# Kernel optimization log

Hardware: AMD Instinct MI355X
Metric: run time of the kernel (lower is better)

The kernel has to match this reference:

```python
import jax, jax.numpy as jnp
import numpy as np

B, L, H, NH = 2, 1024, 768, 12
NE, M, NC, CW = 24, 3, 2, 8
BLOCK, NCLS = 64, 97
OFFSET = 1  # bert cls offset


def setup_inputs() -> dict:
    key = jax.random.key(0)
    ks = jax.random.split(key, 10)
    s = 0.02
    return {
        "sequence_output": jax.random.normal(ks[0], (B, L, H), jnp.float32),
        "attention": jax.random.uniform(ks[1], (B, NH, L, L), jnp.float32),
        "mention_starts": jax.random.randint(ks[2], (B, NE, M), 0, L - 2),
        "coref_starts": jax.random.randint(ks[3], (B, NE, NC), 0, L - CW),
        "W_head": jax.random.normal(ks[4], (H, 2 * H), jnp.float32) * s,
        "b_head": jnp.zeros((H,), jnp.float32),
        "W_tail": jax.random.normal(ks[5], (H, 2 * H), jnp.float32) * s,
        "b_tail": jnp.zeros((H,), jnp.float32),
        "W_proj": jax.random.normal(ks[6], (H, H * BLOCK), jnp.float32) * s,
        "W_cls": jax.random.normal(ks[7], (NCLS, H), jnp.float32) * s,
        "b_cls": jnp.zeros((NCLS,), jnp.float32),
    }


def reference(sequence_output, attention, mention_starts, coref_starts,
              W_head, b_head, W_tail, b_tail, W_proj, W_cls, b_cls):
    # ---- get_hrt (NoGraphConv/NoKGEmbedding => graph feats are zeros; residual=True) ----
    p = mention_starts + OFFSET                              # [B,NE,M]
    bidx = jnp.arange(B)[:, None, None]
    m_emb = sequence_output[bidx, p]                         # [B,NE,M,H]
    # attention[i,:,pos] gathered for every mention -> [B,NE,M,NH,L]
    m_att = attention[bidx, :, p]

    # gated coref: gate_score = mean-over-mentions, sum-over-heads, normalized
    att = m_att.mean(2).sum(2)                               # [B,NE,L]
    gate = att / att.sum(-1, keepdims=True)                  # [B,NE,L]

    widx = coref_starts[..., None] + jnp.arange(CW)          # [B,NE,NC,CW]
    gate_g = jnp.take_along_axis(gate[:, :, None, :], widx, axis=-1)   # [B,NE,NC,CW]
    seq_g = sequence_output[jnp.arange(B)[:, None, None, None], widx]  # [B,NE,NC,CW,H]
    coref_emb = (gate_g[..., None] * seq_g).sum(3)           # [B,NE,NC,H]

    # entity embedding: logsumexp over mentions + gated coref vectors
    e_emb = jax.nn.logsumexp(jnp.concatenate([m_emb, coref_emb], axis=2), axis=2)  # [B,NE,H]
    e_att = m_att.mean(2)                                    # [B,NE,NH,L]

    # head-tail localized context: relu((h_att*t_att).sum(heads)), normalize, mix tokens
    ht = jax.nn.relu(jnp.einsum('behl,bfhl->befl', e_att, e_att))      # [B,NE,NE,L]
    ht = ht / (ht.sum(-1, keepdims=True) + 1e-10)
    rs = jnp.einsum('befl,bld->befd', ht, sequence_output)   # [B,NE,NE,H]

    hs = jnp.broadcast_to(e_emb[:, :, None, :], (B, NE, NE, H))
    ts = jnp.broadcast_to(e_emb[:, None, :, :], (B, NE, NE, H))

    # ---- extractors + grouped bilinear + projection + classifier ----
    zh = jnp.tanh(jnp.concatenate([hs, rs], -1) @ W_head.T + b_head)   # [B,NE,NE,H]
    zt = jnp.tanh(jnp.concatenate([ts, rs], -1) @ W_tail.T + b_tail)
    K = H // BLOCK
    b1 = zh.reshape(B, NE, NE, K, BLOCK)
    b2 = zt.reshape(B, NE, NE, K, BLOCK)
    bl = (b1[..., :, None] * b2[..., None, :]).reshape(B, NE, NE, H * BLOCK)
    feature = bl @ W_proj.T                                  # [B,NE,NE,H] (NoAxialTransformer adds zeros)
    logits = feature @ W_cls.T + b_cls                       # [B,NE,NE,NCLS]
    return logits
```

## Files before the change

### kernel.cpp

```cpp
#include <hip/hip_runtime.h>
#include <math.h>

#define BB   2
#define LL   1024
#define HH   768
#define NHH  12
#define NEE  24
#define MMM  3
#define NCC  2
#define CWW  8
#define BLK  64
#define NCLS 97
#define KB   12
#define HB   49152
#define NCP  128
#define NCT  7
#define NEF  1152

typedef unsigned int uint;
typedef unsigned short ushort;
typedef __attribute__((ext_vector_type(8))) short bf16x8;
typedef __attribute__((ext_vector_type(4))) float f32x4;

__device__ __forceinline__ ushort f2bf(float f) {
    uint u = __float_as_uint(f);
    u += 0x7fffu + ((u >> 16) & 1u);
    return (ushort)(u >> 16);
}

__global__ void k_eatt(const float* __restrict__ att_in, const int* __restrict__ ms,
                       float* __restrict__ e_att) {
    int blk = blockIdx.x;
    int h = blk % NHH;
    int e = (blk / NHH) % NEE;
    int b = blk / (NHH * NEE);
    int base = (b * NEE + e) * MMM;
    int p0 = ms[base + 0] + 1;
    int p1 = ms[base + 1] + 1;
    int p2 = ms[base + 2] + 1;
    const float* r0 = att_in + ((size_t)(b * NHH + h) * LL + p0) * LL;
    const float* r1 = att_in + ((size_t)(b * NHH + h) * LL + p1) * LL;
    const float* r2 = att_in + ((size_t)(b * NHH + h) * LL + p2) * LL;
    float* o = e_att + ((size_t)(b * NEE + e) * NHH + h) * LL;
    for (int l = threadIdx.x; l < LL; l += blockDim.x)
        o[l] = (r0[l] + r1[l] + r2[l]) * (1.f / 3.f);
}

__global__ void k_gate(const float* __restrict__ e_att, float* __restrict__ gate) {
    int be = blockIdx.x;
    __shared__ float att_s[LL];
    __shared__ float red[4];
    const float* ea = e_att + (size_t)be * NHH * LL;
    float lsum = 0.f;
    for (int l = threadIdx.x; l < LL; l += blockDim.x) {
        float a = 0.f;
        for (int h = 0; h < NHH; h++) a += ea[h * LL + l];
        att_s[l] = a;
        lsum += a;
    }
    for (int off = 32; off; off >>= 1) lsum += __shfl_down(lsum, off, 64);
    if ((threadIdx.x & 63) == 0) red[threadIdx.x >> 6] = lsum;
    __syncthreads();
    float inv = 1.f / (red[0] + red[1] + red[2] + red[3]);
    for (int l = threadIdx.x; l < LL; l += blockDim.x)
        gate[(size_t)be * LL + l] = att_s[l] * inv;
}

__global__ void k_eemb(const float* __restrict__ seq, const float* __restrict__ gate,
                       const int* __restrict__ ms, const int* __restrict__ cs,
                       float* __restrict__ e_emb) {
    int be = blockIdx.x;
    int b = be / NEE;
    int p0 = ms[be * MMM + 0] + 1, p1 = ms[be * MMM + 1] + 1, p2 = ms[be * MMM + 2] + 1;
    int c0 = cs[be * NCC + 0], c1 = cs[be * NCC + 1];
    for (int d = threadIdx.x; d < HH; d += blockDim.x) {
        float v0 = seq[((size_t)b * LL + p0) * HH + d];
        float v1 = seq[((size_t)b * LL + p1) * HH + d];
        float v2 = seq[((size_t)b * LL + p2) * HH + d];
        float s0 = 0.f, s1 = 0.f;
        for (int w = 0; w < CWW; w++) {
            s0 += gate[(size_t)be * LL + c0 + w] * seq[((size_t)b * LL + c0 + w) * HH + d];
            s1 += gate[(size_t)be * LL + c1 + w] * seq[((size_t)b * LL + c1 + w) * HH + d];
        }
        float mx = fmaxf(fmaxf(fmaxf(v0, v1), fmaxf(v2, s0)), s1);
        float s = expf(v0 - mx) + expf(v1 - mx) + expf(v2 - mx) + expf(s0 - mx) + expf(s1 - mx);
        e_emb[(size_t)be * HH + d] = logf(s) + mx;
    }
}

__global__ void k_ht(const float* __restrict__ e_att, float* __restrict__ ht) {
    int blk = blockIdx.x;
    int f = blk % NEE;
    int e = (blk / NEE) % NEE;
    int b = blk / (NEE * NEE);
    const float* ea = e_att + (size_t)(b * NEE + e) * NHH * LL;
    const float* fa = e_att + (size_t)(b * NEE + f) * NHH * LL;
    __shared__ float hts[LL];
    __shared__ float red[4];
    float lsum = 0.f;
    for (int l = threadIdx.x; l < LL; l += blockDim.x) {
        float s = 0.f;
        for (int h = 0; h < NHH; h++) s += ea[h * LL + l] * fa[h * LL + l];
        s = fmaxf(s, 0.f);
        hts[l] = s;
        lsum += s;
    }
    for (int off = 32; off; off >>= 1) lsum += __shfl_down(lsum, off, 64);
    if ((threadIdx.x & 63) == 0) red[threadIdx.x >> 6] = lsum;
    __syncthreads();
    float inv = 1.f / (red[0] + red[1] + red[2] + red[3] + 1e-10f);
    for (int l = threadIdx.x; l < LL; l += blockDim.x)
        ht[(size_t)blk * LL + l] = hts[l] * inv;
}

__global__ void k_zrs(float* __restrict__ rs) {
    int i = blockIdx.x * 256 + threadIdx.x;
    rs[i] = 0.f;
}

__global__ void k_rs(const float* __restrict__ seq, const float* __restrict__ ht,
                     float* __restrict__ rs) {
    int m0 = blockIdx.x * 64;
    int n0 = blockIdx.y * 64;
    int b  = blockIdx.z >> 1;
    int k0base = (blockIdx.z & 1) * 512;
    const float* A  = ht  + (size_t)b * 576 * 1024;
    const float* Bm = seq + (size_t)b * 1024 * 768;
    float* C = rs + (size_t)b * 576 * 768;
    __shared__ float As[16][68], Bs[16][68];
    int tx = threadIdx.x & 15, ty = threadIdx.x >> 4;
    int lr = threadIdx.x >> 2;
    int lk = (threadIdx.x & 3) * 4;
    int kr = threadIdx.x >> 4;
    int c4 = (threadIdx.x & 15) * 4;
    float acc[4][4] = {};
    const float* arow = A + (size_t)(m0 + lr) * 1024 + k0base;
    const float* brow = Bm + (size_t)(k0base + kr) * 768 + n0 + c4;
    for (int k0 = 0; k0 < 512; k0 += 16) {
        float4 av = *(const float4*)(arow + k0 + lk);
        float4 bv = *(const float4*)(brow + (size_t)k0 * 768);
        __syncthreads();
        As[lk + 0][lr] = av.x; As[lk + 1][lr] = av.y; As[lk + 2][lr] = av.z; As[lk + 3][lr] = av.w;
        *(float4*)&Bs[kr][c4] = bv;
        __syncthreads();
#pragma unroll
        for (int kk = 0; kk < 16; kk++) {
            float a0 = As[kk][ty * 4 + 0], a1 = As[kk][ty * 4 + 1];
            float a2 = As[kk][ty * 4 + 2], a3 = As[kk][ty * 4 + 3];
            float b0 = Bs[kk][tx * 4 + 0], b1 = Bs[kk][tx * 4 + 1];
            float b2 = Bs[kk][tx * 4 + 2], b3 = Bs[kk][tx * 4 + 3];
            acc[0][0] += a0 * b0; acc[0][1] += a0 * b1; acc[0][2] += a0 * b2; acc[0][3] += a0 * b3;
            acc[1][0] += a1 * b0; acc[1][1] += a1 * b1; acc[1][2] += a1 * b2; acc[1][3] += a1 * b3;
            acc[2][0] += a2 * b0; acc[2][1] += a2 * b1; acc[2][2] += a2 * b2; acc[2][3] += a2 * b3;
            acc[3][0] += a3 * b0; acc[3][1] += a3 * b1; acc[3][2] += a3 * b2; acc[3][3] += a3 * b3;
        }
    }
#pragma unroll
    for (int i = 0; i < 4; i++)
#pragma unroll
        for (int j = 0; j < 4; j++)
            atomicAdd(&C[(size_t)(m0 + ty * 4 + i) * 768 + n0 + tx * 4 + j], acc[i][j]);
}

__global__ void k_hw(const float* __restrict__ e_emb, const float* __restrict__ Wh,
                     const float* __restrict__ Wt, float* __restrict__ hsW,
                     float* __restrict__ tsW) {
    int m2 = blockIdx.x;
    int which = blockIdx.y;
    int chunk = blockIdx.z;
    const float* Wm = which ? Wt : Wh;
    float* outp = which ? tsW : hsW;
    __shared__ float xs[HH];
    const float* x = e_emb + (size_t)m2 * HH;
    for (int j = threadIdx.x; j < HH; j += 256) xs[j] = x[j];
    __syncthreads();
    int lane = threadIdx.x & 63, w = threadIdx.x >> 6;
    int d0 = chunk * 64 + w * 16;
#pragma unroll 4
    for (int i = 0; i < 16; i++) {
        int d = d0 + i;
        const float* wr = Wm + (size_t)d * (2 * HH);
        float s = 0.f;
#pragma unroll
        for (int jj = 0; jj < 12; jj++) s += xs[lane + jj * 64] * wr[lane + jj * 64];
        for (int off = 32; off; off >>= 1) s += __shfl_down(s, off, 64);
        if (lane == 0) outp[(size_t)m2 * HH + d] = s;
    }
}

__global__ void k_rsw(const float* __restrict__ rs, const float* __restrict__ Wh,
                      const float* __restrict__ Wt, float* __restrict__ rsW) {
    int m0 = blockIdx.x * 64, n0 = blockIdx.y * 64;
    __shared__ float As[16][68], Bs[16][68];
    int tx = threadIdx.x & 15, ty = threadIdx.x >> 4;
    int lr = threadIdx.x >> 2;
    int lk = (threadIdx.x & 3) * 4;
    float acc[4][4] = {};
    int n = n0 + lr;
    const float* brow = (n < HH) ? (Wh + (size_t)n * (2 * HH) + HH)
                                 : (Wt + (size_t)(n - HH) * (2 * HH) + HH);
    const float* arow = rs + (size_t)(m0 + lr) * HH;
    for (int k0 = 0; k0 < HH; k0 += 16) {
        float4 av = *(const float4*)(arow + k0 + lk);
        float4 bv = *(const float4*)(brow + k0 + lk);
        __syncthreads();
        As[lk + 0][lr] = av.x; As[lk + 1][lr] = av.y; As[lk + 2][lr] = av.z; As[lk + 3][lr] = av.w;
        Bs[lk + 0][lr] = bv.x; Bs[lk + 1][lr] = bv.y; Bs[lk + 2][lr] = bv.z; Bs[lk + 3][lr] = bv.w;
        __syncthreads();
#pragma unroll
        for (int kk = 0; kk < 16; kk++) {
            float a0 = As[kk][ty * 4 + 0], a1 = As[kk][ty * 4 + 1];
            float a2 = As[kk][ty * 4 + 2], a3 = As[kk][ty * 4 + 3];
            float b0 = Bs[kk][tx * 4 + 0], b1 = Bs[kk][tx * 4 + 1];
            float b2 = Bs[kk][tx * 4 + 2], b3 = Bs[kk][tx * 4 + 3];
            acc[0][0] += a0 * b0; acc[0][1] += a0 * b1; acc[0][2] += a0 * b2; acc[0][3] += a0 * b3;
            acc[1][0] += a1 * b0; acc[1][1] += a1 * b1; acc[1][2] += a1 * b2; acc[1][3] += a1 * b3;
            acc[2][0] += a2 * b0; acc[2][1] += a2 * b1; acc[2][2] += a2 * b2; acc[2][3] += a2 * b3;
            acc[3][0] += a3 * b0; acc[3][1] += a3 * b1; acc[3][2] += a3 * b2; acc[3][3] += a3 * b3;
        }
    }
#pragma unroll
    for (int i = 0; i < 4; i++)
#pragma unroll
        for (int j = 0; j < 4; j++)
            rsW[(size_t)(m0 + ty * 4 + i) * (2 * HH) + n0 + tx * 4 + j] = acc[i][j];
}

__global__ void k_tanh(const float* __restrict__ rsW, const float* __restrict__ hsW,
                       const float* __restrict__ tsW, const float* __restrict__ bh,
                       const float* __restrict__ bt, ushort* __restrict__ zb) {
    size_t i = (size_t)blockIdx.x * 256 + threadIdx.x;
    if (i >= (size_t)NEF * 2 * HH) return;
    int nn = (int)(i % (2 * HH));
    int m = (int)(i / (2 * HH));
    int f = m % NEE;
    int e = (m / NEE) % NEE;
    int b = m / (NEE * NEE);
    float v = rsW[i];
    if (nn < HH) v = tanhf(v + hsW[(size_t)(b * NEE + e) * HH + nn] + bh[nn]);
    else {
        int d = nn - HH;
        v = tanhf(v + tsW[(size_t)(b * NEE + f) * HH + d] + bt[d]);
    }
    zb[i] = f2bf(v);
}

__global__ void k_wcp(const float* __restrict__ Wc, ushort* __restrict__ wcpack) {
    int t = blockIdx.x * 256 + threadIdx.x;
    if (t >= 24 * NCT * 64) return;
    int kc = t / (NCT * 64);
    int r = t % (NCT * 64);
    int ct = r >> 6;
    int lane = r & 63;
    int c = ct * 16 + (lane & 15);
    int k0 = kc * 32 + (lane >> 4) * 8;
    uint u[4] = {0u, 0u, 0u, 0u};
    if (c < NCLS) {
        const float* src = Wc + (size_t)c * HH + k0;
        float4 f0 = *(const float4*)src;
        float4 f1 = *(const float4*)(src + 4);
        u[0] = (uint)f2bf(f0.x) | ((uint)f2bf(f0.y) << 16);
        u[1] = (uint)f2bf(f0.z) | ((uint)f2bf(f0.w) << 16);
        u[2] = (uint)f2bf(f1.x) | ((uint)f2bf(f1.y) << 16);
        u[3] = (uint)f2bf(f1.z) | ((uint)f2bf(f1.w) << 16);
    }
    *(uint4*)(wcpack + (size_t)t * 8) = make_uint4(u[0], u[1], u[2], u[3]);
}

__global__ void k_wf(const float* __restrict__ Wp, const ushort* __restrict__ wcpack,
                     ushort* __restrict__ bpack) {
    int tid = threadIdx.x;
    int lane = tid & 63, w = tid >> 6;
    int r16 = lane & 15, tt = lane >> 4;
    int n0 = blockIdx.x * 64 + w * 16;
    const float* ap = Wp + (size_t)(tt * 8) * HB + n0 + r16;
    const uint4* wb = (const uint4*)wcpack;

    f32x4 acc[NCT];
    f32x4 zero = {0.f, 0.f, 0.f, 0.f};
#pragma unroll
    for (int ct = 0; ct < NCT; ct++) acc[ct] = zero;

    for (int kc = 0; kc < 24; kc++) {
        const float* a0 = ap + (size_t)(kc * 32) * HB;
        float f[8];
#pragma unroll
        for (int j = 0; j < 8; j++) f[j] = a0[(size_t)j * HB];
        union { bf16x8 v; uint u[4]; } a;
#pragma unroll
        for (int q = 0; q < 4; q++)
            a.u[q] = (__float_as_uint(f[2 * q]) >> 16) |
                     (__float_as_uint(f[2 * q + 1]) & 0xFFFF0000u);
#pragma unroll
        for (int ct = 0; ct < NCT; ct++) {
            union { uint4 q; bf16x8 v; } b;
            b.q = wb[(size_t)(kc * NCT + ct) * 64 + lane];
            acc[ct] = __builtin_amdgcn_mfma_f32_16x16x32_bf16(a.v, b.v, acc[ct], 0, 0, 0);
        }
    }
#pragma unroll
    for (int ct = 0; ct < NCT; ct++) {
        int c = ct * 16 + r16;
#pragma unroll
        for (int r = 0; r < 4; r++) {
            int n = n0 + tt * 4 + r;
            bpack[((size_t)(n >> 3) * NCP + c) * 8 + (n & 7)] = f2bf(acc[ct][r]);
        }
    }
}

__global__ void k_init(float* __restrict__ out, const float* __restrict__ bc) {
    int i = blockIdx.x * 256 + threadIdx.x;
    if (i < NEF * NCLS) out[i] = bc[i % NCLS];
}

#define ZTP 88
#define ZHP 48
__global__ __launch_bounds__(256, 2) void k_logits(const ushort* __restrict__ zb,
                                                   const ushort* __restrict__ bpack,
                                                   float* __restrict__ out) {
    __shared__ ushort zhs[64 * ZHP];
    __shared__ ushort zts[64 * ZTP];
    __shared__ ushort Bls[16384];
    int m0 = blockIdx.x * 64;
    int kb = blockIdx.y;
    int kg = kb >> 1;
    int ihalf = (kb & 1) * 32;
    int tid = threadIdx.x;
    int lane = tid & 63, w = tid >> 6;
    int tt = lane >> 4, r16 = lane & 15;
    int wm = (w & 1) * 32, wn = (w >> 1) * 64;

    {
        int row = tid >> 2, c8 = (tid & 3) * 16;
        const ushort* src = zb + (size_t)(m0 + row) * 1536 + 768 + kg * 64 + c8;
        uint4 v0 = *(const uint4*)src;
        uint4 v1 = *(const uint4*)(src + 8);
        *(uint4*)&zts[row * ZTP + c8] = v0;
        *(uint4*)&zts[row * ZTP + c8 + 8] = v1;
    }
    {
        int row = tid >> 2, c8 = (tid & 3) * 8;
        const ushort* src = zb + (size_t)(m0 + row) * 1536 + kg * 64 + ihalf + c8;
        *(uint4*)&zhs[row * ZHP + c8] = *(const uint4*)src;
    }

    f32x4 acc[2][4];
    f32x4 zero = {0.f, 0.f, 0.f, 0.f};
#pragma unroll
    for (int t = 0; t < 2; t++)
#pragma unroll
        for (int n = 0; n < 4; n++) acc[t][n] = zero;

    const char* bbase = (const char*)bpack + (size_t)kb * 2048 * 256;
    for (int g = 0; g < 16; g++) {
        __syncthreads();
        const char* sb = bbase + (size_t)g * 32768;
#pragma unroll
        for (int q = 0; q < 8; q++) {
            int off = (q * 4 + w) * 1024;
            __builtin_amdgcn_global_load_lds(
                (const __attribute__((address_space(1))) void*)(sb + off + lane * 16),
                (__attribute__((address_space(3))) void*)((char*)Bls + off),
                16, 0, 0);
        }
        __syncthreads();
#pragma unroll
        for (int ks = 0; ks < 4; ks++) {
            int s = g * 4 + ks;
            int il = s >> 1;
            int j0 = (s & 1) * 32;
            bf16x8 af[2];
#pragma unroll
            for (int t = 0; t < 2; t++) {
                int row = wm + t * 16 + r16;
                float zhf = __uint_as_float((uint)zhs[row * ZHP + il] << 16);
                union { bf16x8 v; uint u[4]; } zt8, a;
                zt8.v = *(const bf16x8*)&zts[row * ZTP + j0 + tt * 8];
#pragma unroll
                for (int q = 0; q < 4; q++) {
                    uint p = zt8.u[q];
                    uint lo = __float_as_uint(__uint_as_float(p << 16) * zhf);
                    uint hi = __float_as_uint(__uint_as_float(p & 0xFFFF0000u) * zhf);
                    a.u[q] = (lo >> 16) | (hi & 0xFFFF0000u);
                }
                af[t] = a.v;
            }
#pragma unroll
            for (int n = 0; n < 4; n++) {
                bf16x8 bf = *(const bf16x8*)&Bls[(size_t)((ks * 4 + tt) * NCP + wn + n * 16 + r16) * 8];
                acc[0][n] = __builtin_amdgcn_mfma_f32_16x16x32_bf16(af[0], bf, acc[0][n], 0, 0, 0);
                acc[1][n] = __builtin_amdgcn_mfma_f32_16x16x32_bf16(af[1], bf, acc[1][n], 0, 0, 0);
            }
        }
    }
    int rbase = (lane >> 4) * 4;
#pragma unroll
    for (int t = 0; t < 2; t++)
#pragma unroll
        for (int n = 0; n < 4; n++) {
            int c = wn + n * 16 + r16;
            if (c < NCLS) {
                int row = m0 + wm + t * 16 + rbase;
#pragma unroll
                for (int r = 0; r < 4; r++)
                    atomicAdd(&out[(size_t)(row + r) * NCLS + c], acc[t][n][r]);
            }
        }
}

extern "C" void kernel_launch(void* const* d_in, const int* in_sizes, int n_in,
                              void* d_out, int out_size, void* d_ws, size_t ws_size,
                              hipStream_t stream) {
    const float* seq  = (const float*)d_in[0];
    const float* attn = (const float*)d_in[1];
    const int*   ms   = (const int*)d_in[2];
    const int*   cs   = (const int*)d_in[3];
    const float* Wh   = (const float*)d_in[4];
    const float* bh   = (const float*)d_in[5];
    const float* Wt   = (const float*)d_in[6];
    const float* bt   = (const float*)d_in[7];
    const float* Wp   = (const float*)d_in[8];
    const float* Wc   = (const float*)d_in[9];
    const float* bc   = (const float*)d_in[10];
    float* out = (float*)d_out;

    float* w     = (float*)d_ws;
    float* rsW   = w;
    float* regB  = w + 1769472;
    float* e_att = regB;
    float* gate  = e_att + 589824;
    float* ht    = gate + 49152;
    float* rs    = ht + 1179648;
    float* eemb  = rs + 884736;
    float* hsW   = eemb + 36864;
    float* tsW   = hsW + 36864;
    ushort* bpack  = (ushort*)regB;
    ushort* zb     = (ushort*)(regB + 3145728);
    ushort* wcpack = (ushort*)(regB + 4030464);

    k_wcp<<<(24 * NCT * 64 + 255) / 256, 256, 0, stream>>>(Wc, wcpack);
    k_eatt<<<BB * NEE * NHH, 256, 0, stream>>>(attn, ms, e_att);
    k_gate<<<BB * NEE, 256, 0, stream>>>(e_att, gate);
    k_eemb<<<BB * NEE, 256, 0, stream>>>(seq, gate, ms, cs, eemb);
    k_ht<<<NEF, 256, 0, stream>>>(e_att, ht);
    k_zrs<<<(NEF * HH) / 256, 256, 0, stream>>>(rs);
    k_rs<<<dim3(576 / 64, HH / 64, BB * 2), 256, 0, stream>>>(seq, ht, rs);
    k_hw<<<dim3(48, 2, 12), 256, 0, stream>>>(eemb, Wh, Wt, hsW, tsW);
    k_rsw<<<dim3(NEF / 64, 2 * HH / 64), 256, 0, stream>>>(rs, Wh, Wt, rsW);
    k_tanh<<<(NEF * 2 * HH + 255) / 256, 256, 0, stream>>>(rsW, hsW, tsW, bh, bt, zb);
    k_wf<<<HB / 64, 256, 0, stream>>>(Wp, wcpack, bpack);
    k_init<<<(NEF * NCLS + 255) / 256, 256, 0, stream>>>(out, bc);
    k_logits<<<dim3(NEF / 64, 24), 256, 0, stream>>>(zb, bpack, out);
}
```

Before: 490.4 us.

## Fuse small kernels: prep, head attention/gate/emb, mid GEMMs, tanh epilogue

Merges the weight packing, rs zeroing and output bias init into one launch, and combines mention attention averaging, gate normalisation and entity embedding into a single 1024-thread block per entity. The rs GEMM and the hs/ts projections now share one launch, and the tanh/bias/bf16 conversion moves into the epilogue of the rs-weight GEMM, so the rsW intermediate is never written to memory. This removes launch overhead and the gate and rsW round trips through global memory. In exchange it has fewer launches with mixed block roles, and the head kernel runs only 48 large blocks.

```diff
diff --git a/kernel.cpp b/kernel.cpp
--- a/kernel.cpp
+++ b/kernel.cpp
@@ -28,63 +28,89 @@
     return (ushort)(u >> 16);
 }
 
-__global__ void k_eatt(const float* __restrict__ att_in, const int* __restrict__ ms,
-                       float* __restrict__ e_att) {
-    int blk = blockIdx.x;
-    int h = blk % NHH;
-    int e = (blk / NHH) % NEE;
-    int b = blk / (NHH * NEE);
-    int base = (b * NEE + e) * MMM;
+__global__ void k_prep(const float* __restrict__ Wc, ushort* __restrict__ wcpack,
+                       float* __restrict__ rs, float* __restrict__ out,
+                       const float* __restrict__ bc) {
+    int bid = blockIdx.x;
+    if (bid < 42) {
+        int t = bid * 256 + threadIdx.x;
+        if (t >= 24 * NCT * 64) return;
+        int kc = t / (NCT * 64);
+        int r = t % (NCT * 64);
+        int ct = r >> 6;
+        int lane = r & 63;
+        int c = ct * 16 + (lane & 15);
+        int k0 = kc * 32 + (lane >> 4) * 8;
+        uint u[4] = {0u, 0u, 0u, 0u};
+        if (c < NCLS) {
+            const float* src = Wc + (size_t)c * HH + k0;
+            float4 f0 = *(const float4*)src;
+            float4 f1 = *(const float4*)(src + 4);
+            u[0] = (uint)f2bf(f0.x) | ((uint)f2bf(f0.y) << 16);
+            u[1] = (uint)f2bf(f0.z) | ((uint)f2bf(f0.w) << 16);
+            u[2] = (uint)f2bf(f1.x) | ((uint)f2bf(f1.y) << 16);
+            u[3] = (uint)f2bf(f1.z) | ((uint)f2bf(f1.w) << 16);
+        }
+        *(uint4*)(wcpack + (size_t)t * 8) = make_uint4(u[0], u[1], u[2], u[3]);
+    } else if (bid < 42 + 3456) {
+        int i = (bid - 42) * 256 + threadIdx.x;
+        rs[i] = 0.f;
+    } else {
+        int i = (bid - 3498) * 256 + threadIdx.x;
+        if (i < NEF * NCLS) out[i] = bc[i % NCLS];
+    }
+}
+
+__global__ void k_head(const float* __restrict__ att_in, const float* __restrict__ seq,
+                       const int* __restrict__ ms, const int* __restrict__ cs,
+                       float* __restrict__ e_att, float* __restrict__ e_emb) {
+    __shared__ float es[NHH][LL];
+    __shared__ float gs[LL];
+    __shared__ float red[16];
+    int be = blockIdx.x;
+    int b = be / NEE;
+    int base = be * MMM;
     int p0 = ms[base + 0] + 1;
     int p1 = ms[base + 1] + 1;
     int p2 = ms[base + 2] + 1;
-    const float* r0 = att_in + ((size_t)(b * NHH + h) * LL + p0) * LL;
-    const float* r1 = att_in + ((size_t)(b * NHH + h) * LL + p1) * LL;
-    const float* r2 = att_in + ((size_t)(b * NHH + h) * LL + p2) * LL;
-    float* o = e_att + ((size_t)(b * NEE + e) * NHH + h) * LL;
-    for (int l = threadIdx.x; l < LL; l += blockDim.x)
-        o[l] = (r0[l] + r1[l] + r2[l]) * (1.f / 3.f);
-}
-
-__global__ void k_gate(const float* __restrict__ e_att, float* __restrict__ gate) {
-    int be = blockIdx.x;
-    __shared__ float att_s[LL];
-    __shared__ float red[4];
-    const float* ea = e_att + (size_t)be * NHH * LL;
-    float lsum = 0.f;
-    for (int l = threadIdx.x; l < LL; l += blockDim.x) {
-        float a = 0.f;
-        for (int h = 0; h < NHH; h++) a += ea[h * LL + l];
-        att_s[l] = a;
-        lsum += a;
-    }
-    for (int off = 32; off; off >>= 1) lsum += __shfl_down(lsum, off, 64);
-    if ((threadIdx.x & 63) == 0) red[threadIdx.x >> 6] = lsum;
+    int l = threadIdx.x;
+    float* eo = e_att + (size_t)be * NHH * LL;
+#pragma unroll
+    for (int h = 0; h < NHH; h++) {
+        const float* basep = att_in + (size_t)(b * NHH + h) * LL * LL;
+        float v = (basep[(size_t)p0 * LL + l] + basep[(size_t)p1 * LL + l] +
+                   basep[(size_t)p2 * LL + l]) * (1.f / 3.f);
+        es[h][l] = v;
+        eo[h * LL + l] = v;
+    }
     __syncthreads();
-    float inv = 1.f / (red[0] + red[1] + red[2] + red[3]);
-    for (int l = threadIdx.x; l < LL; l += blockDim.x)
-        gate[(size_t)be * LL + l] = att_s[l] * inv;
-}
-
-__global__ void k_eemb(const float* __restrict__ seq, const float* __restrict__ gate,
-                       const int* __restrict__ ms, const int* __restrict__ cs,
-                       float* __restrict__ e_emb) {
-    int be = blockIdx.x;
-    int b = be / NEE;
-    int p0 = ms[be * MMM + 0] + 1, p1 = ms[be * MMM + 1] + 1, p2 = ms[be * MMM + 2] + 1;
-    int c0 = cs[be * NCC + 0], c1 = cs[be * NCC + 1];
-    for (int d = threadIdx.x; d < HH; d += blockDim.x) {
+    float a = 0.f;
+#pragma unroll
+    for (int h = 0; h < NHH; h++) a += es[h][l];
+    float s = a;
+    for (int off = 32; off; off >>= 1) s += __shfl_down(s, off, 64);
+    if ((l & 63) == 0) red[l >> 6] = s;
+    __syncthreads();
+    float tot = 0.f;
+#pragma unroll
+    for (int i = 0; i < 16; i++) tot += red[i];
+    gs[l] = a * (1.f / tot);
+    __syncthreads();
+    if (l < HH) {
+        int d = l;
+        int c0 = cs[be * NCC + 0], c1 = cs[be * NCC + 1];
         float v0 = seq[((size_t)b * LL + p0) * HH + d];
         float v1 = seq[((size_t)b * LL + p1) * HH + d];
         float v2 = seq[((size_t)b * LL + p2) * HH + d];
         float s0 = 0.f, s1 = 0.f;
+#pragma unroll
         for (int w = 0; w < CWW; w++) {
-            s0 += gate[(size_t)be * LL + c0 + w] * seq[((size_t)b * LL + c0 + w) * HH + d];
-            s1 += gate[(size_t)be * LL + c1 + w] * seq[((size_t)b * LL + c1 + w) * HH + d];
+            s0 += gs[c0 + w] * seq[((size_t)b * LL + c0 + w) * HH + d];
+            s1 += gs[c1 + w] * seq[((size_t)b * LL + c1 + w) * HH + d];
         }
         float mx = fmaxf(fmaxf(fmaxf(v0, v1), fmaxf(v2, s0)), s1);
-        float s = expf(v0 - mx) + expf(v1 - mx) + expf(v2 - mx) + expf(s0 - mx) + expf(s1 - mx);
-        e_emb[(size_t)be * HH + d] = logf(s) + mx;
+        float se = expf(v0 - mx) + expf(v1 - mx) + expf(v2 - mx) + expf(s0 - mx) + expf(s1 - mx);
+        e_emb[(size_t)be * HH + d] = logf(se) + mx;
     }
 }
 
@@ -113,83 +139,83 @@
         ht[(size_t)blk * LL + l] = hts[l] * inv;
 }
 
-__global__ void k_zrs(float* __restrict__ rs) {
-    int i = blockIdx.x * 256 + threadIdx.x;
-    rs[i] = 0.f;
-}
-
-__global__ void k_rs(const float* __restrict__ seq, const float* __restrict__ ht,
-                     float* __restrict__ rs) {
-    int m0 = blockIdx.x * 64;
-    int n0 = blockIdx.y * 64;
-    int b  = blockIdx.z >> 1;
-    int k0base = (blockIdx.z & 1) * 512;
-    const float* A  = ht  + (size_t)b * 576 * 1024;
-    const float* Bm = seq + (size_t)b * 1024 * 768;
-    float* C = rs + (size_t)b * 576 * 768;
+__global__ void k_mid(const float* __restrict__ seq, const float* __restrict__ ht,
+                      float* __restrict__ rs, const float* __restrict__ e_emb,
+                      const float* __restrict__ Wh, const float* __restrict__ Wt,
+                      float* __restrict__ hsW, float* __restrict__ tsW) {
     __shared__ float As[16][68], Bs[16][68];
-    int tx = threadIdx.x & 15, ty = threadIdx.x >> 4;
-    int lr = threadIdx.x >> 2;
-    int lk = (threadIdx.x & 3) * 4;
-    int kr = threadIdx.x >> 4;
-    int c4 = (threadIdx.x & 15) * 4;
-    float acc[4][4] = {};
-    const float* arow = A + (size_t)(m0 + lr) * 1024 + k0base;
-    const float* brow = Bm + (size_t)(k0base + kr) * 768 + n0 + c4;
-    for (int k0 = 0; k0 < 512; k0 += 16) {
-        float4 av = *(const float4*)(arow + k0 + lk);
-        float4 bv = *(const float4*)(brow + (size_t)k0 * 768);
+    __shared__ float xs[HH];
+    int bid = blockIdx.x;
+    if (bid < 432) {
+        int m0 = (bid % 9) * 64;
+        int n0 = ((bid / 9) % 12) * 64;
+        int z  = bid / 108;
+        int b  = z >> 1;
+        int k0base = (z & 1) * 512;
+        const float* A  = ht  + (size_t)b * 576 * 1024;
+        const float* Bm = seq + (size_t)b * 1024 * 768;
+        float* C = rs + (size_t)b * 576 * 768;
+        int tx = threadIdx.x & 15, ty = threadIdx.x >> 4;
+        int lr = threadIdx.x >> 2;
+        int lk = (threadIdx.x & 3) * 4;
+        int kr = threadIdx.x >> 4;
+        int c4 = (threadIdx.x & 15) * 4;
+        float acc[4][4] = {};
+        const float* arow = A + (size_t)(m0 + lr) * 1024 + k0base;
+        const float* brow = Bm + (size_t)(k0base + kr) * 768 + n0 + c4;
+        for (int k0 = 0; k0 < 512; k0 += 16) {
+            float4 av = *(const float4*)(arow + k0 + lk);
+            float4 bv = *(const float4*)(brow + (size_t)k0 * 768);
+            __syncthreads();
+            As[lk + 0][lr] = av.x; As[lk + 1][lr] = av.y; As[lk + 2][lr] = av.z; As[lk + 3][lr] = av.w;
+            *(float4*)&Bs[kr][c4] = bv;
+            __syncthreads();
+#pragma unroll
+            for (int kk = 0; kk < 16; kk++) {
+                float a0 = As[kk][ty * 4 + 0], a1 = As[kk][ty * 4 + 1];
+                float a2 = As[kk][ty * 4 + 2], a3 = As[kk][ty * 4 + 3];
+                float b0 = Bs[kk][tx * 4 + 0], b1 = Bs[kk][tx * 4 + 1];
+                float b2 = Bs[kk][tx * 4 + 2], b3 = Bs[kk][tx * 4 + 3];
+                acc[0][0] += a0 * b0; acc[0][1] += a0 * b1; acc[0][2] += a0 * b2; acc[0][3] += a0 * b3;
+                acc[1][0] += a1 * b0; acc[1][1] += a1 * b1; acc[1][2] += a1 * b2; acc[1][3] += a1 * b3;
+                acc[2][0] += a2 * b0; acc[2][1] += a2 * b1; acc[2][2] += a2 * b2; acc[2][3] += a2 * b3;
+                acc[3][0] += a3 * b0; acc[3][1] += a3 * b1; acc[3][2] += a3 * b2; acc[3][3] += a3 * b3;
+            }
+        }
+#pragma unroll
+        for (int i = 0; i < 4; i++)
+#pragma unroll
+            for (int j = 0; j < 4; j++)
+                atomicAdd(&C[(size_t)(m0 + ty * 4 + i) * 768 + n0 + tx * 4 + j], acc[i][j]);
+    } else {
+        int r = bid - 432;
+        int m2 = r % 48;
+        int which = (r / 48) & 1;
+        int chunk = r / 96;
+        const float* Wm = which ? Wt : Wh;
+        float* outp = which ? tsW : hsW;
+        const float* x = e_emb + (size_t)m2 * HH;
+        for (int j = threadIdx.x; j < HH; j += 256) xs[j] = x[j];
         __syncthreads();
-        As[lk + 0][lr] = av.x; As[lk + 1][lr] = av.y; As[lk + 2][lr] = av.z; As[lk + 3][lr] = av.w;
-        *(float4*)&Bs[kr][c4] = bv;
-        __syncthreads();
-#pragma unroll
-        for (int kk = 0; kk < 16; kk++) {
-            float a0 = As[kk][ty * 4 + 0], a1 = As[kk][ty * 4 + 1];
-            float a2 = As[kk][ty * 4 + 2], a3 = As[kk][ty * 4 + 3];
-            float b0 = Bs[kk][tx * 4 + 0], b1 = Bs[kk][tx * 4 + 1];
-            float b2 = Bs[kk][tx * 4 + 2], b3 = Bs[kk][tx * 4 + 3];
-            acc[0][0] += a0 * b0; acc[0][1] += a0 * b1; acc[0][2] += a0 * b2; acc[0][3] += a0 * b3;
-            acc[1][0] += a1 * b0; acc[1][1] += a1 * b1; acc[1][2] += a1 * b2; acc[1][3] += a1 * b3;
-            acc[2][0] += a2 * b0; acc[2][1] += a2 * b1; acc[2][2] += a2 * b2; acc[2][3] += a2 * b3;
-            acc[3][0] += a3 * b0; acc[3][1] += a3 * b1; acc[3][2] += a3 * b2; acc[3][3] += a3 * b3;
-        }
-    }
-#pragma unroll
-    for (int i = 0; i < 4; i++)
-#pragma unroll
-        for (int j = 0; j < 4; j++)
-            atomicAdd(&C[(size_t)(m0 + ty * 4 + i) * 768 + n0 + tx * 4 + j], acc[i][j]);
-}
-
-__global__ void k_hw(const float* __restrict__ e_emb, const float* __restrict__ Wh,
-                     const float* __restrict__ Wt, float* __restrict__ hsW,
-                     float* __restrict__ tsW) {
-    int m2 = blockIdx.x;
-    int which = blockIdx.y;
-    int chunk = blockIdx.z;
-    const float* Wm = which ? Wt : Wh;
-    float* outp = which ? tsW : hsW;
-    __shared__ float xs[HH];
-    const float* x = e_emb + (size_t)m2 * HH;
-    for (int j = threadIdx.x; j < HH; j += 256) xs[j] = x[j];
-    __syncthreads();
-    int lane = threadIdx.x & 63, w = threadIdx.x >> 6;
-    int d0 = chunk * 64 + w * 16;
+        int lane = threadIdx.x & 63, w = threadIdx.x >> 6;
+        int d0 = chunk * 64 + w * 16;
 #pragma unroll 4
-    for (int i = 0; i < 16; i++) {
-        int d = d0 + i;
-        const float* wr = Wm + (size_t)d * (2 * HH);
-        float s = 0.f;
-#pragma unroll
-        for (int jj = 0; jj < 12; jj++) s += xs[lane + jj * 64] * wr[lane + jj * 64];
-        for (int off = 32; off; off >>= 1) s += __shfl_down(s, off, 64);
-        if (lane == 0) outp[(size_t)m2 * HH + d] = s;
+        for (int i = 0; i < 16; i++) {
+            int d = d0 + i;
+            const float* wr = Wm + (size_t)d * (2 * HH);
+            float s = 0.f;
+#pragma unroll
+            for (int jj = 0; jj < 12; jj++) s += xs[lane + jj * 64] * wr[lane + jj * 64];
+            for (int off = 32; off; off >>= 1) s += __shfl_down(s, off, 64);
+            if (lane == 0) outp[(size_t)m2 * HH + d] = s;
+        }
     }
 }
 
 __global__ void k_rsw(const float* __restrict__ rs, const float* __restrict__ Wh,
-                      const float* __restrict__ Wt, float* __restrict__ rsW) {
+                      const float* __restrict__ Wt, const float* __restrict__ hsW,
+                      const float* __restrict__ tsW, const float* __restrict__ bh,
+                      const float* __restrict__ bt, ushort* __restrict__ zb) {
     int m0 = blockIdx.x * 64, n0 = blockIdx.y * 64;
     __shared__ float As[16][68], Bs[16][68];
     int tx = threadIdx.x & 15, ty = threadIdx.x >> 4;
@@ -219,52 +245,24 @@
             acc[3][0] += a3 * b0; acc[3][1] += a3 * b1; acc[3][2] += a3 * b2; acc[3][3] += a3 * b3;
         }
     }
-#pragma unroll
-    for (int i = 0; i < 4; i++)
-#pragma unroll
-        for (int j = 0; j < 4; j++)
-            rsW[(size_t)(m0 + ty * 4 + i) * (2 * HH) + n0 + tx * 4 + j] = acc[i][j];
-}
-
-__global__ void k_tanh(const float* __restrict__ rsW, const float* __restrict__ hsW,
-                       const float* __restrict__ tsW, const float* __restrict__ bh,
-                       const float* __restrict__ bt, ushort* __restrict__ zb) {
-    size_t i = (size_t)blockIdx.x * 256 + threadIdx.x;
-    if (i >= (size_t)NEF * 2 * HH) return;
-    int nn = (int)(i % (2 * HH));
-    int m = (int)(i / (2 * HH));
-    int f = m % NEE;
-    int e = (m / NEE) % NEE;
-    int b = m / (NEE * NEE);
-    float v = rsW[i];
-    if (nn < HH) v = tanhf(v + hsW[(size_t)(b * NEE + e) * HH + nn] + bh[nn]);
-    else {
-        int d = nn - HH;
-        v = tanhf(v + tsW[(size_t)(b * NEE + f) * HH + d] + bt[d]);
-    }
-    zb[i] = f2bf(v);
-}
-
-__global__ void k_wcp(const float* __restrict__ Wc, ushort* __restrict__ wcpack) {
-    int t = blockIdx.x * 256 + threadIdx.x;
-    if (t >= 24 * NCT * 64) return;
-    int kc = t / (NCT * 64);
-    int r = t % (NCT * 64);
-    int ct = r >> 6;
-    int lane = r & 63;
-    int c = ct * 16 + (lane & 15);
-    int k0 = kc * 32 + (lane >> 4) * 8;
-    uint u[4] = {0u, 0u, 0u, 0u};
-    if (c < NCLS) {
-        const float* src = Wc + (size_t)c * HH + k0;
-        float4 f0 = *(const float4*)src;
-        float4 f1 = *(const float4*)(src + 4);
-        u[0] = (uint)f2bf(f0.x) | ((uint)f2bf(f0.y) << 16);
-        u[1] = (uint)f2bf(f0.z) | ((uint)f2bf(f0.w) << 16);
-        u[2] = (uint)f2bf(f1.x) | ((uint)f2bf(f1.y) << 16);
-        u[3] = (uint)f2bf(f1.z) | ((uint)f2bf(f1.w) << 16);
-    }
-    *(uint4*)(wcpack + (size_t)t * 8) = make_uint4(u[0], u[1], u[2], u[3]);
+    bool isHead = (n0 < HH);
+#pragma unroll
+    for (int i = 0; i < 4; i++) {
+        int m = m0 + ty * 4 + i;
+        int bb = m / 576;
+        int rr = m % 576;
+        int e = rr / NEE, f = rr % NEE;
+        const float* addrow = isHead ? (hsW + (size_t)(bb * NEE + e) * HH)
+                                     : (tsW + (size_t)(bb * NEE + f) * HH);
+        const float* bias = isHead ? bh : bt;
+#pragma unroll
+        for (int j = 0; j < 4; j++) {
+            int nn = n0 + tx * 4 + j;
+            int d = isHead ? nn : (nn - HH);
+            float v = tanhf(acc[i][j] + addrow[d] + bias[d]);
+            zb[(size_t)m * (2 * HH) + nn] = f2bf(v);
+        }
+    }
 }
 
 __global__ void k_wf(const float* __restrict__ Wp, const ushort* __restrict__ wcpack,
@@ -307,11 +305,6 @@
             bpack[((size_t)(n >> 3) * NCP + c) * 8 + (n & 7)] = f2bf(acc[ct][r]);
         }
     }
-}
-
-__global__ void k_init(float* __restrict__ out, const float* __restrict__ bc) {
-    int i = blockIdx.x * 256 + threadIdx.x;
-    if (i < NEF * NCLS) out[i] = bc[i % NCLS];
 }
 
 #define ZTP 88
@@ -426,30 +419,21 @@
     float* out = (float*)d_out;
 
     float* w     = (float*)d_ws;
-    float* rsW   = w;
-    float* regB  = w + 1769472;
-    float* e_att = regB;
-    float* gate  = e_att + 589824;
-    float* ht    = gate + 49152;
+    float* e_att = w;
+    float* ht    = e_att + 589824;
     float* rs    = ht + 1179648;
     float* eemb  = rs + 884736;
     float* hsW   = eemb + 36864;
     float* tsW   = hsW + 36864;
-    ushort* bpack  = (ushort*)regB;
-    ushort* zb     = (ushort*)(regB + 3145728);
-    ushort* wcpack = (ushort*)(regB + 4030464);
-
-    k_wcp<<<(24 * NCT * 64 + 255) / 256, 256, 0, stream>>>(Wc, wcpack);
-    k_eatt<<<BB * NEE * NHH, 256, 0, stream>>>(attn, ms, e_att);
-    k_gate<<<BB * NEE, 256, 0, stream>>>(e_att, gate);
-    k_eemb<<<BB * NEE, 256, 0, stream>>>(seq, gate, ms, cs, eemb);
+    ushort* bpack  = (ushort*)w;
+    ushort* zb     = (ushort*)(w + 3145728);
+    ushort* wcpack = (ushort*)(w + 4030464);
+
+    k_prep<<<3935, 256, 0, stream>>>(Wc, wcpack, rs, out, bc);
+    k_head<<<BB * NEE, 1024, 0, stream>>>(attn, seq, ms, cs, e_att, eemb);
     k_ht<<<NEF, 256, 0, stream>>>(e_att, ht);
-    k_zrs<<<(NEF * HH) / 256, 256, 0, stream>>>(rs);
-    k_rs<<<dim3(576 / 64, HH / 64, BB * 2), 256, 0, stream>>>(seq, ht, rs);
-    k_hw<<<dim3(48, 2, 12), 256, 0, stream>>>(eemb, Wh, Wt, hsW, tsW);
-    k_rsw<<<dim3(NEF / 64, 2 * HH / 64), 256, 0, stream>>>(rs, Wh, Wt, rsW);
-    k_tanh<<<(NEF * 2 * HH + 255) / 256, 256, 0, stream>>>(rsW, hsW, tsW, bh, bt, zb);
+    k_mid<<<432 + 1152, 256, 0, stream>>>(seq, ht, rs, eemb, Wh, Wt, hsW, tsW);
+    k_rsw<<<dim3(NEF / 64, 2 * HH / 64), 256, 0, stream>>>(rs, Wh, Wt, hsW, tsW, bh, bt, zb);
     k_wf<<<HB / 64, 256, 0, stream>>>(Wp, wcpack, bpack);
-    k_init<<<(NEF * NCLS + 255) / 256, 256, 0, stream>>>(out, bc);
     k_logits<<<dim3(NEF / 64, 24), 256, 0, stream>>>(zb, bpack, out);
 }
```

Measured after the change: 461.4 us. -5.9%, faster.
